# Optimization experiments

Hardware: AMD Instinct MI355X
Metric: run time of the kernel (lower is better)

The kernel has to match this reference:

```python
import jax, jax.numpy as jnp
import numpy as np

BATCH, L = 2, 1024
D_MODEL, D_INNER, D_STATE, DT_RANK, K = 2048, 4096, 16, 128, 4


def setup_inputs() -> dict:
    key = jax.random.key(0)
    ks = jax.random.split(key, 9)
    g = lambda i, shape, s: jax.random.normal(ks[i], shape, jnp.float32) * s
    A_log = jnp.log(jnp.broadcast_to(jnp.arange(1, D_STATE + 1, dtype=jnp.float32),
                                     (D_INNER, D_STATE)))
    return {
        "hidden_states": g(0, (BATCH, L, D_MODEL), 1.0),
        "W_in": g(1, (2 * D_INNER, D_MODEL), 0.02),
        "conv_w": g(2, (D_INNER, K), 0.2),
        "conv_b": g(3, (D_INNER,), 0.02),
        "W_x": g(4, (DT_RANK + 2 * D_STATE, D_INNER), 0.02),
        "W_dt": g(5, (D_INNER, DT_RANK), 0.02),
        "b_dt": g(6, (D_INNER,), 0.02),
        "A_log": A_log,
        "D": jnp.ones((D_INNER,), jnp.float32),
        "W_out": g(7, (D_MODEL, D_INNER), 0.02),
        "b_out": g(8, (D_MODEL,), 0.02),
    }


def reference(hidden_states, W_in, conv_w, conv_b, W_x, W_dt, b_dt, A_log, D, W_out, b_out):
    b, l, _ = hidden_states.shape
    # in_proj -> (b, 2*d_inner, l), split into x and gate z
    xz = jnp.einsum('bld,ed->bel', hidden_states, W_in)
    x, z = jnp.split(xz, 2, axis=1)                      # each (b, d_inner, l)
    # conv_state = F.pad(x, (d_conv - l, 0)): keeps the last d_conv timesteps
    conv_state = x[:, :, -K:]
    # causal depthwise conv1d (left pad K-1) + SiLU
    xc = jax.lax.conv_general_dilated(
        x, conv_w[:, None, :], window_strides=(1,), padding=[(K - 1, 0)],
        feature_group_count=D_INNER, dimension_numbers=('NCH', 'OIH', 'NCH'))
    xc = jax.nn.silu(xc + conv_b[None, :, None])         # (b, d_inner, l)
    # x_proj -> dt / B / C
    x_dbl = jnp.einsum('bdl,ed->ble', xc, W_x)           # (b, l, dt_rank+2n)
    dt, Bm, Cm = jnp.split(x_dbl, [DT_RANK, DT_RANK + D_STATE], axis=-1)
    dt = jnp.einsum('blr,dr->bdl', dt, W_dt)             # (b, d_inner, l), no bias here
    delta = jax.nn.softplus(dt + b_dt[None, :, None])    # dt_proj bias folded into softplus
    A = -jnp.exp(A_log)                                  # (d_inner, d_state)

    def step(state, inp):                                # state: (b, d_inner, d_state)
        d_t, b_t, c_t, u_t = inp                         # (b,d), (b,n), (b,n), (b,d)
        dA = jnp.exp(d_t[..., None] * A)                 # (b, d, n)
        state = dA * state + (d_t * u_t)[..., None] * b_t[:, None, :]
        y_t = jnp.einsum('bdn,bn->bd', state, c_t)
        return state, y_t

    xs = (delta.transpose(2, 0, 1),                      # (l, b, d)
          Bm.transpose(1, 0, 2),                         # (l, b, n)
          Cm.transpose(1, 0, 2),
          xc.transpose(2, 0, 1))
    init = jnp.zeros((b, D_INNER, D_STATE), delta.dtype)
    last_state, ys = jax.lax.scan(step, init, xs)
    y = ys.transpose(1, 2, 0) + D[None, :, None] * xc    # (b, d_inner, l) skip term
    y = y * jax.nn.silu(z)                               # gating
    out = jnp.einsum('bdl,ed->ble', y, W_out) + b_out    # (b, l, d_model)
    return out, conv_state, last_state
```

## Files before the change

### kernel.cpp

```cpp
#include <hip/hip_runtime.h>
#include <stdint.h>
#include <stddef.h>

typedef __bf16 bf16;
typedef __attribute__((ext_vector_type(8))) __bf16 bf16x8;
typedef __attribute__((ext_vector_type(4))) float floatx4;

#define GAS __attribute__((address_space(1)))
#define LAS __attribute__((address_space(3)))

__device__ __forceinline__ void async16(const void* g, void* l) {
  __builtin_amdgcn_global_load_lds((const GAS void*)g, (LAS void*)l, 16, 0, 0);
}

__device__ __forceinline__ bf16x8 cvt8(const float* p) {
  floatx4 a = *(const floatx4*)p;
  floatx4 b = *(const floatx4*)(p + 4);
  bf16x8 r;
  r[0] = (bf16)a[0]; r[1] = (bf16)a[1]; r[2] = (bf16)a[2]; r[3] = (bf16)a[3];
  r[4] = (bf16)b[0]; r[5] = (bf16)b[1]; r[6] = (bf16)b[2]; r[7] = (bf16)b[3];
  return r;
}

__global__ __launch_bounds__(512, 2) void gemm256_8p(
    const bf16* __restrict__ A, const bf16* __restrict__ B,
    bf16* __restrict__ C, int M, int N, int K, int lda, int ldb) {
  __shared__ __attribute__((aligned(16))) bf16 SA[2][2][8192];
  __shared__ __attribute__((aligned(16))) bf16 SB[2][2][8192];

  const int tid = threadIdx.x;
  const int wave = tid >> 6;
  const int lane = tid & 63;
  const int lr = lane & 15;
  const int kg = lane >> 4;
  const int wm = (wave >> 2) * 128;
  const int wn = (wave & 3) * 64;

  const int tilesM = M >> 8;
  const int tm = blockIdx.x % tilesM;
  const int tn = blockIdx.x / tilesM;
  const int rowBase = tm * 256;
  const int colBase = tn * 256;

  const int srow = tid >> 2;
  const int ske = (tid & 3) << 3;
  const int skel = ske ^ (((srow >> 1) & 3) << 3);
  const size_t aRow0 = (size_t)(rowBase + srow) * lda;
  const size_t aRow1 = aRow0 + (size_t)128 * lda;
  const size_t bRow0 = (size_t)(colBase + srow) * ldb;
  const size_t bRow1 = bRow0 + (size_t)128 * ldb;

  const int NT = K >> 6;

  const int keSh = (kg << 3) ^ (((lr >> 1) & 3) << 3);

  floatx4 acc[8][4] = {};
  bf16x8 af0[4], af1[4], bgA[4], bgB[4];

  auto stA = [&](int buf, int kh, int kt) {
    const int gk = kt * 64 + kh * 32 + skel;
    bf16* d = &SA[buf][kh][0];
    async16(A + aRow0 + gk, d + tid * 8);
    async16(A + aRow1 + gk, d + 4096 + tid * 8);
  };
  auto stB = [&](int buf, int kh, int kt) {
    const int gk = kt * 64 + kh * 32 + skel;
    bf16* d = &SB[buf][kh][0];
    async16(B + bRow0 + gk, d + tid * 8);
    async16(B + bRow1 + gk, d + 4096 + tid * 8);
  };

#define RD_B(DST, BUF, KH)                                                     \
  _Pragma("unroll") for (int n = 0; n < 4; ++n)                                \
      DST[n] = *(const bf16x8*)&SB[BUF][KH][(wn + n * 16 + lr) * 32 + keSh];
#define RD_A(DST, BUF, KH, MH)                                                 \
  _Pragma("unroll") for (int m = 0; m < 4; ++m)                                \
      DST[m] =                                                                 \
          *(const bf16x8*)&SA[BUF][KH][(wm + ((MH)*4 + m) * 16 + lr) * 32 +    \
                                       keSh];

  stB(0, 0, 0); stA(0, 0, 0); stB(0, 1, 0); stA(0, 1, 0);
  asm volatile("s_waitcnt vmcnt(0)" ::: "memory");
  __builtin_amdgcn_s_barrier();
  stB(1, 0, 1); stA(1, 0, 1); stB(1, 1, 1);
  RD_B(bgA, 0, 0);
  RD_A(af0, 0, 0, 0);

#define PH(RDS, CNT, STG, BGR, AFR, MH, VM)                                    \
  {                                                                            \
    RDS;                                                                       \
    STG;                                                                       \
    __builtin_amdgcn_s_barrier();                                              \
    asm volatile("s_waitcnt lgkmcnt(" #CNT ")" ::: "memory");                  \
    __builtin_amdgcn_sched_barrier(0);                                         \
    __builtin_amdgcn_s_setprio(1);                                             \
    _Pragma("unroll") for (int m = 0; m < 4; ++m)                              \
      _Pragma("unroll") for (int n = 0; n < 4; ++n)                            \
          acc[(MH)*4 + m][n] = __builtin_amdgcn_mfma_f32_16x16x32_bf16(        \
              AFR[m], BGR[n], acc[(MH)*4 + m][n], 0, 0, 0);                    \
    __builtin_amdgcn_s_setprio(0);                                             \
    __builtin_amdgcn_sched_barrier(0);                                         \
    if constexpr (VM) asm volatile("s_waitcnt vmcnt(8)" ::: "memory");         \
    __builtin_amdgcn_s_barrier();                                              \
  }

  for (int it = 0; it < (NT >> 1); ++it) {
    const int T0 = it * 2;
    const int T1 = T0 + 1;
    const int s1 = (T0 + 2 < NT) ? T0 + 2 : NT - 1;
    const int s2 = (T1 + 2 < NT) ? T1 + 2 : NT - 1;

    PH(RD_A(af1, 0, 0, 1), 4, stA(1, 1, T1), bgA, af0, 0, true)
    PH(RD_B(bgB, 0, 1); RD_A(af0, 0, 1, 0), 8, stB(0, 0, s1), bgA, af1, 1,
       false)
    PH(RD_A(af1, 0, 1, 1), 4, stA(0, 0, s1), bgB, af0, 0, true)
    PH(RD_B(bgA, 1, 0); RD_A(af0, 1, 0, 0), 8, stB(0, 1, s1), bgB, af1, 1,
       false)
    PH(RD_A(af1, 1, 0, 1), 4, stA(0, 1, s1), bgA, af0, 0, true)
    PH(RD_B(bgB, 1, 1); RD_A(af0, 1, 1, 0), 8, stB(1, 0, s2), bgA, af1, 1,
       false)
    PH(RD_A(af1, 1, 1, 1), 4, stA(1, 0, s2), bgB, af0, 0, true)
    PH(RD_B(bgA, 0, 0); RD_A(af0, 0, 0, 0), 8, stB(1, 1, s2), bgB, af1, 1,
       false)
  }
#undef PH
#undef RD_A
#undef RD_B

  asm volatile("s_waitcnt vmcnt(0) lgkmcnt(0)" ::: "memory");

#pragma unroll
  for (int m = 0; m < 8; ++m) {
#pragma unroll
    for (int n = 0; n < 4; ++n) {
      const int col = colBase + wn + n * 16 + lr;
#pragma unroll
      for (int r = 0; r < 4; ++r) {
        const int row = rowBase + wm + m * 16 + kg * 4 + r;
        C[(size_t)row * N + col] = (bf16)acc[m][n][r];
      }
    }
  }
}

template <int EPI, int AF, int BF, int TM>
__global__ __launch_bounds__(256, 4) void gemm_bt(
    const void* __restrict__ Aptr, const void* __restrict__ Bptr,
    void* __restrict__ Cout, const float* __restrict__ bias,
    int M, int N, int K, int lda, int ldb) {
  __shared__ bf16 As[TM * 32];
  __shared__ bf16 Bs[128 * 32];
  const int tid = threadIdx.x;

  const int rowBase = blockIdx.x * TM;
  const int colBase = blockIdx.y * 128;
  const int kLen = K / gridDim.z;
  const int k0 = blockIdx.z * kLen;
  const int kIters = kLen / 32;

  const int sRow = tid >> 2;
  const int sCol = (tid & 3) << 3;
  const int wave = tid >> 6;
  const int lane = tid & 63;
  constexpr int MI = 4;
  constexpr int NJ = (TM == 128) ? 4 : 2;
  const int wm = (TM == 128) ? ((wave >> 1) << 6) : 0;
  const int wn = (TM == 128) ? ((wave & 1) << 6) : (wave << 5);
  const int lr = lane & 15;
  const int kg = lane >> 4;

  floatx4 acc[MI][NJ] = {};

  for (int kt = 0; kt < kIters; ++kt) {
    const int kk = k0 + kt * 32;
    __syncthreads();
    if constexpr (AF) {
      const float* pa =
          (const float*)Aptr + (size_t)(rowBase + sRow) * lda + kk + sCol;
      *(bf16x8*)&As[tid * 8] = cvt8(pa);
      if constexpr (TM == 128)
        *(bf16x8*)&As[2048 + tid * 8] = cvt8(pa + (size_t)64 * lda);
    } else {
      const bf16* pa =
          (const bf16*)Aptr + (size_t)(rowBase + sRow) * lda + kk + sCol;
      async16(pa, &As[tid * 8]);
      if constexpr (TM == 128)
        async16(pa + (size_t)64 * lda, &As[2048 + tid * 8]);
    }
    if constexpr (BF) {
      const float* pb =
          (const float*)Bptr + (size_t)(colBase + sRow) * ldb + kk + sCol;
      *(bf16x8*)&Bs[tid * 8] = cvt8(pb);
      *(bf16x8*)&Bs[2048 + tid * 8] = cvt8(pb + (size_t)64 * ldb);
    } else {
      const bf16* pb =
          (const bf16*)Bptr + (size_t)(colBase + sRow) * ldb + kk + sCol;
      async16(pb, &Bs[tid * 8]);
      async16(pb + (size_t)64 * ldb, &Bs[2048 + tid * 8]);
    }
    __syncthreads();

    bf16x8 af[MI], bg[NJ];
#pragma unroll
    for (int i = 0; i < MI; ++i)
      af[i] = *(const bf16x8*)&As[(wm + i * 16 + lr) * 32 + kg * 8];
#pragma unroll
    for (int j = 0; j < NJ; ++j)
      bg[j] = *(const bf16x8*)&Bs[(wn + j * 16 + lr) * 32 + kg * 8];
#pragma unroll
    for (int i = 0; i < MI; ++i)
#pragma unroll
      for (int j = 0; j < NJ; ++j)
        acc[i][j] = __builtin_amdgcn_mfma_f32_16x16x32_bf16(af[i], bg[j],
                                                            acc[i][j], 0, 0, 0);
  }

#pragma unroll
  for (int i = 0; i < MI; ++i) {
#pragma unroll
    for (int j = 0; j < NJ; ++j) {
      const int col = colBase + wn + j * 16 + lr;
      float bv = 0.f;
      if constexpr (EPI == 2 || EPI == 3) bv = bias[col];
#pragma unroll
      for (int r = 0; r < 4; ++r) {
        const int row = rowBase + wm + i * 16 + kg * 4 + r;
        const size_t idx = (size_t)row * N + col;
        float v = acc[i][j][r];
        if constexpr (EPI == 0) {
          ((bf16*)Cout)[idx] = (bf16)v;
        } else if constexpr (EPI == 1) {
          atomicAdd((float*)Cout + idx, v);
        } else if constexpr (EPI == 2) {
          v += bv;
          const float t = __expf(v);
          const float sp = (v > 20.f) ? v : __logf(1.f + t);
          ((bf16*)Cout)[idx] = (bf16)sp;
        } else if constexpr (EPI == 3) {
          ((float*)Cout)[idx] = v + bv;
        } else {
          ((float*)Cout)[(size_t)blockIdx.z * 524288 + idx] = v;
        }
      }
    }
  }
}

__global__ __launch_bounds__(256) void reduce_xdbl(
    const float* __restrict__ part, float* __restrict__ xdbl) {
  const size_t i4 = ((size_t)blockIdx.x * 256 + threadIdx.x) * 4;
  floatx4 s = {};
#pragma unroll
  for (int z = 0; z < 8; ++z) {
    const floatx4 v = *(const floatx4*)&part[(size_t)z * 524288 + i4];
    s[0] += v[0]; s[1] += v[1]; s[2] += v[2]; s[3] += v[3];
  }
  *(floatx4*)&xdbl[i4] = s;
}

#define PC0 524288UL
#define PC1 2621440UL
#define PC2 2686976UL
#define PC3 3735552UL
#define PC4 3866624UL
__global__ __launch_bounds__(256) void prep_all(
    const float* __restrict__ h, const float* __restrict__ wi,
    const float* __restrict__ wd, const float* __restrict__ wo,
    const float* __restrict__ wx, bf16* __restrict__ hb,
    bf16* __restrict__ wib, bf16* __restrict__ wdb, bf16* __restrict__ wob,
    bf16* __restrict__ wxp) {
  const size_t c = (size_t)blockIdx.x * 256 + threadIdx.x;
  if (c < PC0) {
    const size_t e = c * 8;
    *(bf16x8*)&hb[e] = cvt8(&h[e]);
  } else if (c < PC1) {
    const size_t e = (c - PC0) * 8;
    *(bf16x8*)&wib[e] = cvt8(&wi[e]);
  } else if (c < PC2) {
    const size_t e = (c - PC1) * 8;
    *(bf16x8*)&wdb[e] = cvt8(&wd[e]);
  } else if (c < PC3) {
    const size_t e = (c - PC2) * 8;
    *(bf16x8*)&wob[e] = cvt8(&wo[e]);
  } else if (c < PC4) {
    const size_t e = (c - PC3) * 8;
    if ((e >> 12) < 160) {
      *(bf16x8*)&wxp[e] = cvt8(&wx[e]);
    } else {
      bf16x8 z = {};
      *(bf16x8*)&wxp[e] = z;
    }
  }
}

__global__ void wxpad_prep(const float* __restrict__ Wx,
                           bf16* __restrict__ WXPAD) {
  const int idx = blockIdx.x * 256 + threadIdx.x;
  const int row = idx >> 12;
  WXPAD[idx] = (row < 160) ? (bf16)Wx[idx] : (bf16)0.f;
}

__global__ void conv_kernel(const bf16* __restrict__ XZ,
                            const float* __restrict__ conv_w,
                            const float* __restrict__ conv_b,
                            bf16* __restrict__ XC,
                            float* __restrict__ outConv) {
  const int idx = blockIdx.x * 256 + threadIdx.x;
  const int d = idx & 4095;
  const int row = idx >> 12;
  const int l = row & 1023;
  float acc = conv_b[d];
#pragma unroll
  for (int k = 0; k < 4; ++k) {
    if (l - 3 + k >= 0)
      acc += conv_w[d * 4 + k] * (float)XZ[(size_t)(row - 3 + k) * 8192 + d];
  }
  const float s = acc / (1.f + __expf(-acc));
  XC[(size_t)row * 4096 + d] = (bf16)s;
  if (idx < 32768) {
    const int k = idx & 3;
    const int dd = (idx >> 2) & 4095;
    const int b = idx >> 14;
    outConv[idx] = (float)XZ[(size_t)(b * 1024 + 1020 + k) * 8192 + dd];
  }
}

#define NCH 32
#define CLEN 32
#define LOG2E 1.44269504088896f

__global__ __launch_bounds__(256) void scan_phase1(
    const bf16* __restrict__ DELTA, const bf16* __restrict__ XC,
    const float* __restrict__ XDBL, const float* __restrict__ A_log,
    bf16* __restrict__ P, bf16* __restrict__ Lc) {
  const int bd = blockIdx.x * 256 + threadIdx.x;
  const int c = blockIdx.y;
  const int b = bd >> 12;
  const int d = bd & 4095;
  float A2[16], st[16], p[16];
#pragma unroll
  for (int n = 0; n < 16; ++n) {
    A2[n] = -__expf(A_log[d * 16 + n]) * LOG2E;
    st[n] = 0.f;
    p[n] = 1.f;
  }
  size_t row = (size_t)b * 1024 + (size_t)c * CLEN;
  for (int t = 0; t < CLEN; ++t, ++row) {
    const float dlt = (float)DELTA[row * 4096 + d];
    const float u = (float)XC[row * 4096 + d];
    const float* __restrict__ Bp = XDBL + row * 256 + 128;
    const float du = dlt * u;
#pragma unroll
    for (int n = 0; n < 16; ++n) {
      const float dA = exp2f(dlt * A2[n]);
      st[n] = dA * st[n] + du * Bp[n];
      p[n] *= dA;
    }
  }
  const size_t o = ((size_t)c * 8192 + bd) * 16;
  bf16x8 pk[2], lk[2];
#pragma unroll
  for (int n = 0; n < 16; ++n) {
    pk[n >> 3][n & 7] = (bf16)p[n];
    lk[n >> 3][n & 7] = (bf16)st[n];
  }
  *(bf16x8*)&P[o] = pk[0];
  *(bf16x8*)&P[o + 8] = pk[1];
  *(bf16x8*)&Lc[o] = lk[0];
  *(bf16x8*)&Lc[o + 8] = lk[1];
}

__global__ __launch_bounds__(64) void scan_phase2(
    const bf16* __restrict__ P, const bf16* __restrict__ Lc,
    float* __restrict__ In, float* __restrict__ lastOut) {
  const int bd = blockIdx.x * 64 + threadIdx.x;
  float st[16] = {};
  for (int c = 0; c < NCH; ++c) {
    const size_t o = ((size_t)c * 8192 + bd) * 16;
    const bf16x8 p0 = *(const bf16x8*)&P[o];
    const bf16x8 p1 = *(const bf16x8*)&P[o + 8];
    const bf16x8 l0 = *(const bf16x8*)&Lc[o];
    const bf16x8 l1 = *(const bf16x8*)&Lc[o + 8];
    floatx4 w[4];
#pragma unroll
    for (int n = 0; n < 16; ++n) w[n >> 2][n & 3] = st[n];
#pragma unroll
    for (int q = 0; q < 4; ++q) *(floatx4*)&In[o + q * 4] = w[q];
#pragma unroll
    for (int n = 0; n < 8; ++n) {
      st[n] = (float)p0[n] * st[n] + (float)l0[n];
      st[8 + n] = (float)p1[n] * st[8 + n] + (float)l1[n];
    }
  }
  const int b = bd >> 12;
  const int d = bd & 4095;
#pragma unroll
  for (int n = 0; n < 16; ++n)
    lastOut[(size_t)b * 65536 + d * 16 + n] = st[n];
}

__global__ __launch_bounds__(256) void scan_phase3(
    const bf16* __restrict__ DELTA, const bf16* __restrict__ XC,
    const bf16* __restrict__ XZ, const float* __restrict__ XDBL,
    const float* __restrict__ A_log, const float* __restrict__ Dp,
    const float* __restrict__ In, bf16* __restrict__ Y) {
  const int bd = blockIdx.x * 256 + threadIdx.x;
  const int c = blockIdx.y;
  const int b = bd >> 12;
  const int d = bd & 4095;
  float A2[16], st[16];
  const size_t o = ((size_t)c * 8192 + bd) * 16;
#pragma unroll
  for (int q = 0; q < 4; ++q) {
    const floatx4 v = *(const floatx4*)&In[o + q * 4];
#pragma unroll
    for (int j = 0; j < 4; ++j) st[q * 4 + j] = v[j];
  }
#pragma unroll
  for (int n = 0; n < 16; ++n)
    A2[n] = -__expf(A_log[d * 16 + n]) * LOG2E;
  const float Dd = Dp[d];
  size_t row = (size_t)b * 1024 + (size_t)c * CLEN;
  for (int t = 0; t < CLEN; ++t, ++row) {
    const float dlt = (float)DELTA[row * 4096 + d];
    const float u = (float)XC[row * 4096 + d];
    const float z = (float)XZ[row * 8192 + 4096 + d];
    const float* __restrict__ Bp = XDBL + row * 256 + 128;
    const float du = dlt * u;
    float y = 0.f;
#pragma unroll
    for (int n = 0; n < 16; ++n) {
      const float dA = exp2f(dlt * A2[n]);
      st[n] = dA * st[n] + du * Bp[n];
      y += st[n] * Bp[16 + n];
    }
    const float sig = 1.f / (1.f + __expf(-z));
    Y[row * 4096 + d] = (bf16)((y + Dd * u) * (z * sig));
  }
}

#define OFF_XZ 0UL
#define OFF_XC 33554432UL
#define OFF_DELTA 50331648UL
#define OFF_Y 83886080UL
#define OFF_XDBL 100663296UL
#define OFF_WXPAD 103284736UL
#define OFF_P 105381888UL
#define OFF_L 113770496UL
#define OFF_HBF 122159104UL
#define OFF_WINBF 130547712UL
#define OFF_WDTBF 164102144UL
#define OFF_WOUTBF 165150720UL
#define WS_NEED_CAST 181927936UL

extern "C" void kernel_launch(void* const* d_in, const int* in_sizes, int n_in,
                              void* d_out, int out_size, void* d_ws,
                              size_t ws_size, hipStream_t stream) {
  const float* hidden = (const float*)d_in[0];
  const float* W_in = (const float*)d_in[1];
  const float* conv_w = (const float*)d_in[2];
  const float* conv_b = (const float*)d_in[3];
  const float* W_x = (const float*)d_in[4];
  const float* W_dt = (const float*)d_in[5];
  const float* b_dt = (const float*)d_in[6];
  const float* A_log = (const float*)d_in[7];
  const float* Dvec = (const float*)d_in[8];
  const float* W_out = (const float*)d_in[9];
  const float* b_out = (const float*)d_in[10];

  char* ws = (char*)d_ws;
  bf16* XZ = (bf16*)(ws + OFF_XZ);
  bf16* XC = (bf16*)(ws + OFF_XC);
  bf16* DELTA = (bf16*)(ws + OFF_DELTA);
  float* PART = (float*)(ws + OFF_DELTA + 16777216UL);
  bf16* Y = (bf16*)(ws + OFF_Y);
  float* XDBL = (float*)(ws + OFF_XDBL);
  bf16* WXPAD = (bf16*)(ws + OFF_WXPAD);
  bf16* P = (bf16*)(ws + OFF_P);
  bf16* Lc = (bf16*)(ws + OFF_L);

  float* out = (float*)d_out;
  float* out_conv = out + 4194304;
  float* out_last = out + 4227072;
  float* In = out;

  const bool castOK = ws_size >= WS_NEED_CAST;
  if (castOK) {
    bf16* HBF = (bf16*)(ws + OFF_HBF);
    bf16* WINBF = (bf16*)(ws + OFF_WINBF);
    bf16* WDTBF = (bf16*)(ws + OFF_WDTBF);
    bf16* WOUTBF = (bf16*)(ws + OFF_WOUTBF);
    prep_all<<<15104, 256, 0, stream>>>(hidden, W_in, W_dt, W_out, W_x, HBF,
                                        WINBF, WDTBF, WOUTBF, WXPAD);
    gemm256_8p<<<dim3(256), 512, 0, stream>>>(HBF, WINBF, XZ, 2048, 8192,
                                              2048, 2048, 2048);
    conv_kernel<<<32768, 256, 0, stream>>>(XZ, conv_w, conv_b, XC, out_conv);
    gemm_bt<4, 0, 0, 64><<<dim3(32, 2, 8), 256, 0, stream>>>(
        XC, WXPAD, PART, nullptr, 2048, 256, 4096, 4096, 4096);
    reduce_xdbl<<<512, 256, 0, stream>>>(PART, XDBL);
    gemm_bt<2, 1, 0, 64><<<dim3(32, 32, 1), 256, 0, stream>>>(
        XDBL, WDTBF, DELTA, b_dt, 2048, 4096, 128, 256, 128);
    scan_phase1<<<dim3(32, NCH), 256, 0, stream>>>(DELTA, XC, XDBL, A_log, P,
                                                   Lc);
    scan_phase2<<<128, 64, 0, stream>>>(P, Lc, In, out_last);
    scan_phase3<<<dim3(32, NCH), 256, 0, stream>>>(DELTA, XC, XZ, XDBL, A_log,
                                                   Dvec, In, Y);
    gemm_bt<3, 0, 0, 64><<<dim3(32, 16, 1), 256, 0, stream>>>(
        Y, WOUTBF, out, b_out, 2048, 2048, 4096, 4096, 4096);
  } else {
    wxpad_prep<<<4096, 256, 0, stream>>>(W_x, WXPAD);
    gemm_bt<0, 1, 1, 128><<<dim3(16, 64, 1), 256, 0, stream>>>(
        hidden, W_in, XZ, nullptr, 2048, 8192, 2048, 2048, 2048);
    conv_kernel<<<32768, 256, 0, stream>>>(XZ, conv_w, conv_b, XC, out_conv);
    gemm_bt<4, 0, 0, 64><<<dim3(32, 2, 8), 256, 0, stream>>>(
        XC, WXPAD, PART, nullptr, 2048, 256, 4096, 4096, 4096);
    reduce_xdbl<<<512, 256, 0, stream>>>(PART, XDBL);
    gemm_bt<2, 1, 1, 64><<<dim3(32, 32, 1), 256, 0, stream>>>(
        XDBL, W_dt, DELTA, b_dt, 2048, 4096, 128, 256, 128);
    scan_phase1<<<dim3(32, NCH), 256, 0, stream>>>(DELTA, XC, XDBL, A_log, P,
                                                   Lc);
    scan_phase2<<<128, 64, 0, stream>>>(P, Lc, In, out_last);
    scan_phase3<<<dim3(32, NCH), 256, 0, stream>>>(DELTA, XC, XZ, XDBL, A_log,
                                                   Dvec, In, Y);
    gemm_bt<3, 0, 1, 64><<<dim3(32, 16, 1), 256, 0, stream>>>(
        Y, W_out, out, b_out, 2048, 2048, 4096, 4096, 4096);
  }
}
```

Measured before the change: 501.8 us.

## Split-K the output projection into two slabs and deepen in_proj prefetch

The output projection GEMM now runs with a K-split of 2 into float slabs in workspace, followed by a reduce kernel that sums both slabs and adds the bias. This doubles the block count so more CUs are busy on a 2048x2048x4096 GEMM. The cost is an extra kernel launch and the write and read of 32 MB of partials. Separately, the 256-tile in_proj GEMM issues the second stage's loads before the initial wait, and its vmcnt waits move to fewer phases with a tighter count, so more global loads stay in flight.

```diff
diff --git a/kernel.cpp b/kernel.cpp
--- a/kernel.cpp
+++ b/kernel.cpp
@@ -80,9 +80,9 @@
                                        keSh];
 
   stB(0, 0, 0); stA(0, 0, 0); stB(0, 1, 0); stA(0, 1, 0);
+  stB(1, 0, 1); stA(1, 0, 1); stB(1, 1, 1);
   asm volatile("s_waitcnt vmcnt(0)" ::: "memory");
   __builtin_amdgcn_s_barrier();
-  stB(1, 0, 1); stA(1, 0, 1); stB(1, 1, 1);
   RD_B(bgA, 0, 0);
   RD_A(af0, 0, 0, 0);
 
@@ -100,7 +100,7 @@
               AFR[m], BGR[n], acc[(MH)*4 + m][n], 0, 0, 0);                    \
     __builtin_amdgcn_s_setprio(0);                                             \
     __builtin_amdgcn_sched_barrier(0);                                         \
-    if constexpr (VM) asm volatile("s_waitcnt vmcnt(8)" ::: "memory");         \
+    if constexpr (VM) asm volatile("s_waitcnt vmcnt(2)" ::: "memory");         \
     __builtin_amdgcn_s_barrier();                                              \
   }
 
@@ -110,18 +110,18 @@
     const int s1 = (T0 + 2 < NT) ? T0 + 2 : NT - 1;
     const int s2 = (T1 + 2 < NT) ? T1 + 2 : NT - 1;
 
-    PH(RD_A(af1, 0, 0, 1), 4, stA(1, 1, T1), bgA, af0, 0, true)
+    PH(RD_A(af1, 0, 0, 1), 4, stA(1, 1, T1), bgA, af0, 0, false)
     PH(RD_B(bgB, 0, 1); RD_A(af0, 0, 1, 0), 8, stB(0, 0, s1), bgA, af1, 1,
        false)
-    PH(RD_A(af1, 0, 1, 1), 4, stA(0, 0, s1), bgB, af0, 0, true)
+    PH(RD_A(af1, 0, 1, 1), 4, stA(0, 0, s1), bgB, af0, 0, false)
     PH(RD_B(bgA, 1, 0); RD_A(af0, 1, 0, 0), 8, stB(0, 1, s1), bgB, af1, 1,
-       false)
-    PH(RD_A(af1, 1, 0, 1), 4, stA(0, 1, s1), bgA, af0, 0, true)
+       true)
+    PH(RD_A(af1, 1, 0, 1), 4, stA(0, 1, s1), bgA, af0, 0, false)
     PH(RD_B(bgB, 1, 1); RD_A(af0, 1, 1, 0), 8, stB(1, 0, s2), bgA, af1, 1,
        false)
-    PH(RD_A(af1, 1, 1, 1), 4, stA(1, 0, s2), bgB, af0, 0, true)
+    PH(RD_A(af1, 1, 1, 1), 4, stA(1, 0, s2), bgB, af0, 0, false)
     PH(RD_B(bgA, 0, 0); RD_A(af0, 0, 0, 0), 8, stB(1, 1, s2), bgB, af1, 1,
-       false)
+       true)
   }
 #undef PH
 #undef RD_A
@@ -238,8 +238,10 @@
           ((bf16*)Cout)[idx] = (bf16)sp;
         } else if constexpr (EPI == 3) {
           ((float*)Cout)[idx] = v + bv;
+        } else if constexpr (EPI == 4) {
+          ((float*)Cout)[(size_t)blockIdx.z * 524288 + idx] = v;
         } else {
-          ((float*)Cout)[(size_t)blockIdx.z * 524288 + idx] = v;
+          ((float*)Cout)[(size_t)blockIdx.z * 4194304 + idx] = v;
         }
       }
     }
@@ -256,6 +258,21 @@
     s[0] += v[0]; s[1] += v[1]; s[2] += v[2]; s[3] += v[3];
   }
   *(floatx4*)&xdbl[i4] = s;
+}
+
+__global__ __launch_bounds__(256) void reduce_out(
+    const float* __restrict__ part, const float* __restrict__ bias,
+    float* __restrict__ outp) {
+  const size_t i4 = ((size_t)blockIdx.x * 256 + threadIdx.x) * 4;
+  const floatx4 a = *(const floatx4*)&part[i4];
+  const floatx4 b = *(const floatx4*)&part[4194304 + i4];
+  const floatx4 bv = *(const floatx4*)&bias[i4 & 2047];
+  floatx4 s;
+  s[0] = a[0] + b[0] + bv[0];
+  s[1] = a[1] + b[1] + bv[1];
+  s[2] = a[2] + b[2] + bv[2];
+  s[3] = a[3] + b[3] + bv[3];
+  *(floatx4*)&outp[i4] = s;
 }
 
 #define PC0 524288UL
@@ -473,6 +490,7 @@
   bf16* XC = (bf16*)(ws + OFF_XC);
   bf16* DELTA = (bf16*)(ws + OFF_DELTA);
   float* PART = (float*)(ws + OFF_DELTA + 16777216UL);
+  float* SLAB3 = (float*)(ws + OFF_DELTA);
   bf16* Y = (bf16*)(ws + OFF_Y);
   float* XDBL = (float*)(ws + OFF_XDBL);
   bf16* WXPAD = (bf16*)(ws + OFF_WXPAD);
@@ -505,8 +523,9 @@
     scan_phase2<<<128, 64, 0, stream>>>(P, Lc, In, out_last);
     scan_phase3<<<dim3(32, NCH), 256, 0, stream>>>(DELTA, XC, XZ, XDBL, A_log,
                                                    Dvec, In, Y);
-    gemm_bt<3, 0, 0, 64><<<dim3(32, 16, 1), 256, 0, stream>>>(
-        Y, WOUTBF, out, b_out, 2048, 2048, 4096, 4096, 4096);
+    gemm_bt<5, 0, 0, 64><<<dim3(32, 16, 2), 256, 0, stream>>>(
+        Y, WOUTBF, SLAB3, nullptr, 2048, 2048, 4096, 4096, 4096);
+    reduce_out<<<4096, 256, 0, stream>>>(SLAB3, b_out, out);
   } else {
     wxpad_prep<<<4096, 256, 0, stream>>>(W_x, WXPAD);
     gemm_bt<0, 1, 1, 128><<<dim3(16, 64, 1), 256, 0, stream>>>(
```

New measurement: 492.2 us. No clear change (-1.9%).
